# Kernel tuning notes

Hardware: AMD Instinct MI355X
Metric: run time of the kernel (lower is better)

## Reference

```python
import jax, jax.numpy as jnp
import numpy as np
from jax import lax

C = 32          # channel_num
DG = 8          # deformable_groups
K = 9           # 3x3 deformable kernel taps
B, H, W = 4, 192, 192


def conv2d(x, w, b, pad):
    y = lax.conv_general_dilated(x, w, (1, 1), [(pad, pad), (pad, pad)],
                                 dimension_numbers=("NCHW", "OIHW", "NCHW"))
    return y + b[None, :, None, None]


def deform_conv2d(x, offset, mask, w, b):
    """Modulated deformable conv v2, 3x3 kernel, stride 1, pad 1, dilation 1.

    x:      [B, C, H, W]
    offset: [B, 2*DG*K, H, W]  laid out as cat(o1, o2): first DG*K = dy, next = dx
    mask:   [B, DG*K, H, W]    (already sigmoided)
    w:      [Cout, C, 3, 3], b: [Cout]
    """
    Bn, Cn, Hn, Wn = x.shape
    Cg = Cn // DG
    off = offset.reshape(Bn, 2, DG, K, Hn, Wn)
    dy, dx = off[:, 0], off[:, 1]                     # [B, DG, K, H, W]
    m = mask.reshape(Bn, DG, K, Hn, Wn)

    ky = jnp.repeat(jnp.arange(3) - 1, 3).astype(x.dtype)  # [K]
    kx = jnp.tile(jnp.arange(3) - 1, 3).astype(x.dtype)    # [K]
    iy = jnp.arange(Hn, dtype=x.dtype)
    ix = jnp.arange(Wn, dtype=x.dtype)
    py = dy + ky[None, None, :, None, None] + iy[None, None, None, :, None]
    px = dx + kx[None, None, :, None, None] + ix[None, None, None, None, :]

    y0 = jnp.floor(py)
    x0 = jnp.floor(px)
    wy = py - y0    # frac weights
    wx = px - x0

    x_flat = x.reshape(Bn, DG, Cg, Hn * Wn)

    def gather(yc, xc):
        valid = (yc >= 0) & (yc < Hn) & (xc >= 0) & (xc < Wn)
        yi = jnp.clip(yc, 0, Hn - 1).astype(jnp.int32)
        xi = jnp.clip(xc, 0, Wn - 1).astype(jnp.int32)
        idx = (yi * Wn + xi).reshape(Bn, DG, 1, K * Hn * Wn)
        v = jnp.take_along_axis(x_flat, jnp.broadcast_to(idx, (Bn, DG, Cg, K * Hn * Wn)), axis=3)
        v = v.reshape(Bn, DG, Cg, K, Hn, Wn)
        return v * valid[:, :, None].astype(x.dtype)

    v00 = gather(y0, x0)
    v01 = gather(y0, x0 + 1)
    v10 = gather(y0 + 1, x0)
    v11 = gather(y0 + 1, x0 + 1)
    wyb = wy[:, :, None]  # [B, DG, 1, K, H, W]
    wxb = wx[:, :, None]
    sampled = ((1 - wyb) * (1 - wxb) * v00 + (1 - wyb) * wxb * v01
               + wyb * (1 - wxb) * v10 + wyb * wxb * v11)
    sampled = sampled * m[:, :, None]                 # modulate
    sampled = sampled.reshape(Bn, Cn, K, Hn, Wn)      # DG*Cg == C, contiguous
    out = jnp.einsum('oik,bikhw->bohw', w.reshape(w.shape[0], Cn, K), sampled)
    return out + b[None, :, None, None]


def setup_inputs() -> dict:
    key = jax.random.key(0)
    ks = jax.random.split(key, 14)
    f = lambda k, shp, s=1.0: jax.random.normal(k, shp, dtype=jnp.float32) * s
    return {
        "img_ref": f(ks[0], (B, C, H, W)),
        "img": f(ks[1], (B, C, H, W)),
        "conv1_w": f(ks[2], (C, 2 * C, 1, 1), 0.05),
        "conv1_b": f(ks[3], (C,), 0.05),
        "conv2a_w": f(ks[4], (C, C, 3, 3), 0.05),
        "conv2a_b": f(ks[5], (C,), 0.05),
        "conv2b_w": f(ks[6], (C, C, 3, 3), 0.05),
        "conv2b_b": f(ks[7], (C,), 0.05),
        "off_w": f(ks[8], (3 * DG * K, C, 3, 3), 0.01),
        "off_b": f(ks[9], (3 * DG * K,), 0.01),
        "dcn_w": f(ks[10], (C, C, 3, 3), 0.05),
        "dcn_b": f(ks[11], (C,), 0.05),
    }


def reference(img_ref, img, conv1_w, conv1_b, conv2a_w, conv2a_b,
              conv2b_w, conv2b_b, off_w, off_b, dcn_w, dcn_b):
    img_cat = conv2d(jnp.concatenate([img_ref, img], axis=1), conv1_w, conv1_b, 0)
    feat = conv2d(conv2d(img_cat, conv2a_w, conv2a_b, 1), conv2b_w, conv2b_b, 1)
    # DCNv2Pack: offsets/mask from feat, deformable sampling on img
    co = conv2d(feat, off_w, off_b, 1)                # [B, 3*DG*K, H, W]
    o1, o2, mask = jnp.split(co, 3, axis=1)
    offset = jnp.concatenate([o1, o2], axis=1)
    mask = jax.nn.sigmoid(mask)
    return deform_conv2d(img, offset, mask, dcn_w, dcn_b)
```

## Files before the change

### kernel.cpp

```cpp
#include <hip/hip_runtime.h>

#define Hc   192
#define Wc   192
#define HWc  (Hc * Wc)
#define NPIX (4 * HWc)
#define Hp   194
#define Wp   256
#define PLANE (Hp * Wp)

typedef float f32x4 __attribute__((ext_vector_type(4)));
typedef float f32x2 __attribute__((ext_vector_type(2)));
typedef __bf16 bf16x8 __attribute__((ext_vector_type(8)));
typedef unsigned short u16;
typedef unsigned int u32;

#define WF_BO    0
#define WF_B1    224
#define WF_B2A   256
#define WF_B2B   288
#define WF_BD    320
#define FR1_U    0
#define FRA_U    2048
#define FRB_U    11264
#define FRO_U    20480
#define FRD_U    84992
#define FRAG_U_TOT 94208
#define FRAG_BYTE 1408
#define T0_BYTE  (FRAG_BYTE + FRAG_U_TOT * 2)
#define T1_BYTE  (T0_BYTE + NPIX * 32 * 2)
#define IMG_BYTE (T1_BYTE + NPIX * 32 * 2)
#define IMG_SZ   ((size_t)4 * 8 * PLANE * 4 * 2)

__device__ __forceinline__ u16 f2bf(float f) {
    u32 u = __float_as_uint(f);
    u32 r = u + 0x7fffu + ((u >> 16) & 1u);
    return (u16)(r >> 16);
}
__device__ __forceinline__ float bf2f(u16 v) {
    return __uint_as_float(((u32)v) << 16);
}
__device__ __forceinline__ u32 cvtpk(float a, float b) {
    u32 r;
    asm("v_cvt_pk_bf16_f32 %0, %1, %2" : "=v"(r) : "v"(a), "v"(b));
    return r;
}
__device__ __forceinline__ f32x2 unpk(u32 h) {
    return f32x2{__uint_as_float(h << 16), __uint_as_float(h & 0xffff0000u)};
}

__global__ __launch_bounds__(256) void prep_k(
    const float* __restrict__ w1,  const float* __restrict__ b1,
    const float* __restrict__ w2a, const float* __restrict__ b2a,
    const float* __restrict__ w2b, const float* __restrict__ b2b,
    const float* __restrict__ wo,  const float* __restrict__ bo,
    const float* __restrict__ wd,  const float* __restrict__ bd,
    float* __restrict__ wsf, u16* __restrict__ frag)
{
    int i = blockIdx.x * 256 + threadIdx.x;
    if (i < 224)      { wsf[WF_BO + i]  = (i < 216) ? bo[i] : 0.f; return; }
    if (i < 256)      { wsf[WF_B1  + i - 224] = b1[i - 224];  return; }
    if (i < 288)      { wsf[WF_B2A + i - 256] = b2a[i - 256]; return; }
    if (i < 320)      { wsf[WF_B2B + i - 288] = b2b[i - 288]; return; }
    if (i < 352)      { wsf[WF_BD  + i - 320] = bd[i - 320];  return; }
    int fi = i - 352;
    if (fi < 2048) {
        int s = fi >> 10, l = (fi >> 3) & 63, j = fi & 7;
        int nt = (fi >> 9) & 1;
        int o = nt * 16 + (l & 15);
        int ci = s * 32 + ((l >> 4) << 3) + j;
        frag[FR1_U + fi] = f2bf(w1[o * 64 + ci]);
        return;
    }
    fi -= 2048;
    if (fi < 9216) {
        int s = fi / 1024, r = fi - s * 1024;
        int nt = r >> 9, l = (r >> 3) & 63, j = r & 7;
        int o = nt * 16 + (l & 15);
        int ci = ((l >> 4) << 3) + j;
        frag[FRA_U + fi] = f2bf(w2a[(o * 32 + ci) * 9 + s]);
        return;
    }
    fi -= 9216;
    if (fi < 9216) {
        int s = fi / 1024, r = fi - s * 1024;
        int nt = r >> 9, l = (r >> 3) & 63, j = r & 7;
        int o = nt * 16 + (l & 15);
        int ci = ((l >> 4) << 3) + j;
        frag[FRB_U + fi] = f2bf(w2b[(o * 32 + ci) * 9 + s]);
        return;
    }
    fi -= 9216;
    if (fi < 64512) {
        int s = fi / 7168, r = fi - s * 7168;
        int nt = r >> 9, l = (r >> 3) & 63, j = r & 7;
        int o = nt * 16 + (l & 15);
        int ci = ((l >> 4) << 3) + j;
        frag[FRO_U + fi] = f2bf((o < 216) ? wo[(o * 32 + ci) * 9 + s] : 0.f);
        return;
    }
    fi -= 64512;
    if (fi < 9216) {
        int k = fi / 1024, r = fi - k * 1024;
        int nt = r >> 9, l = (r >> 3) & 63, j = r & 7;
        int o = nt * 16 + (l & 15);
        int ci = ((l >> 4) << 3) + j;
        frag[FRD_U + fi] = f2bf(wd[o * 288 + ci * 9 + k]);
        return;
    }
}

__global__ __launch_bounds__(256) void conv1x1_mfma_k(
    const float* __restrict__ f0, const float* __restrict__ f1,
    const u16* __restrict__ wfrag, const float* __restrict__ bias,
    u16* __restrict__ y, u16* __restrict__ dump)
{
    constexpr int M_BLK = 128;
    const int tid = threadIdx.x, lane = tid & 63, wv = tid >> 6;
    const int bid = blockIdx.x;
    const int swz = (bid & 7) * (gridDim.x >> 3) + (bid >> 3);
    const int m0 = swz * M_BLK;
    const int b = m0 / HWc, hwb = m0 - b * HWc;
    const int rm = wv * 32;

    __shared__ uint4 At4[512];

    int pxA[2], hA[2], wA[2], kgA[2];
#pragma unroll
    for (int it = 0; it < 2; ++it) {
        int st = it * 256 + tid;
        int rowl = ((st >> 6) << 4) | (st & 15);
        kgA[it] = (st >> 4) & 3;
        pxA[it] = rowl;
        int hwp = hwb + rowl;
        hA[it] = hwp / Wc;
        wA[it] = hwp - hA[it] * Wc;
    }

    f32x4 acc[2][2];
#pragma unroll
    for (int mf = 0; mf < 2; ++mf)
#pragma unroll
        for (int nf = 0; nf < 2; ++nf)
            acc[mf][nf] = f32x4{0.f, 0.f, 0.f, 0.f};

    for (int s = 0; s < 2; ++s) {
        const float* fs = (s == 0) ? f0 : f1;
#pragma unroll
        for (int it = 0; it < 2; ++it) {
            const float* pl = fs + ((size_t)b * 32 + kgA[it] * 8) * HWc + (hwb + pxA[it]);
            u32 p0, p1, p2, p3;
            {
                u32 a0 = f2bf(pl[0 * HWc]), a1 = f2bf(pl[1 * HWc]);
                u32 a2 = f2bf(pl[2 * HWc]), a3 = f2bf(pl[3 * HWc]);
                u32 a4 = f2bf(pl[4 * HWc]), a5 = f2bf(pl[5 * HWc]);
                u32 a6 = f2bf(pl[6 * HWc]), a7 = f2bf(pl[7 * HWc]);
                p0 = a0 | (a1 << 16); p1 = a2 | (a3 << 16);
                p2 = a4 | (a5 << 16); p3 = a6 | (a7 << 16);
            }
            uint4 v = {p0, p1, p2, p3};
            if (s == 1) {
                size_t base = (((size_t)(b * 8 + kgA[it] * 2)) * PLANE
                               + (size_t)(hA[it] + 1) * Wp + (wA[it] + 2)) * 4;
                *(uint2*)(dump + base) = uint2{p0, p1};
                *(uint2*)(dump + base + (size_t)PLANE * 4) = uint2{p2, p3};
            }
            At4[it * 256 + tid] = v;
        }
        __syncthreads();

        bf16x8 aF[2];
#pragma unroll
        for (int mf = 0; mf < 2; ++mf)
            aF[mf] = __builtin_bit_cast(bf16x8, At4[((rm >> 4) + mf) * 64 + lane]);
#pragma unroll
        for (int nf = 0; nf < 2; ++nf) {
            bf16x8 bF = __builtin_bit_cast(
                bf16x8, *(const uint4*)(wfrag + (((size_t)s * 2 + nf) * 64 + lane) * 8));
#pragma unroll
            for (int mf = 0; mf < 2; ++mf)
                acc[mf][nf] = __builtin_amdgcn_mfma_f32_16x16x32_bf16(aF[mf], bF, acc[mf][nf], 0, 0, 0);
        }
        __syncthreads();
    }

#pragma unroll
    for (int nf = 0; nf < 2; ++nf) {
        int o = nf * 16 + (lane & 15);
        float bs = bias[o];
#pragma unroll
        for (int mf = 0; mf < 2; ++mf) {
#pragma unroll
            for (int r = 0; r < 4; ++r) {
                int m = m0 + rm + mf * 16 + ((lane >> 4) << 2) + r;
                y[(size_t)m * 32 + o] = f2bf(acc[mf][nf][r] + bs);
            }
        }
    }
}

__global__ __launch_bounds__(256, 4) void conv3x3h_k(
    const u16* __restrict__ src,
    const u16* __restrict__ wfrag,
    const float* __restrict__ bias,
    u16* __restrict__ dst)
{
    const int tid = threadIdx.x, lane = tid & 63, wv = tid >> 6;
    const int bid = blockIdx.x;
    const int swz = (bid & 7) * (gridDim.x >> 3) + (bid >> 3);
    const int m0 = swz * 64;
    const int b = m0 / HWc, hwb = m0 - b * HWc;
    const int h0 = hwb / Wc, w0 = hwb - h0 * Wc;

    __shared__ u16 xt[198 * 32];

#pragma unroll
    for (int it = 0; it < 4; ++it) {
        int t = it * 256 + tid;
        if (t < 792) {
            int s = t >> 2, c = t & 3;
            int ry = s / 66, cx = s - ry * 66;
            int row = h0 + ry - 1, col = w0 + cx - 1;
            uint4 v = {0u, 0u, 0u, 0u};
            if (((unsigned)row < (unsigned)Hc) && ((unsigned)col < (unsigned)Wc))
                v = *(const uint4*)(src + ((size_t)(b * HWc + row * Wc + col)) * 32 + c * 8);
            *(uint4*)(xt + (size_t)t * 8) = v;
        }
    }
    __syncthreads();

    f32x4 acc0 = {0.f, 0.f, 0.f, 0.f};
    f32x4 acc1 = {0.f, 0.f, 0.f, 0.f};
    const int r0 = wv * 16 + (lane & 15);
    const int kg8 = (lane >> 4) * 8;
#pragma unroll
    for (int kyi = 0; kyi < 3; ++kyi) {
#pragma unroll
        for (int kxi = 0; kxi < 3; ++kxi) {
            const int s9 = kyi * 3 + kxi;
            bf16x8 aF = __builtin_bit_cast(bf16x8,
                *(const uint4*)(xt + (size_t)(kyi * 66 + r0 + kxi) * 32 + kg8));
            bf16x8 bF0 = __builtin_bit_cast(bf16x8,
                *(const uint4*)(wfrag + (((size_t)s9 * 2 + 0) * 64 + lane) * 8));
            bf16x8 bF1 = __builtin_bit_cast(bf16x8,
                *(const uint4*)(wfrag + (((size_t)s9 * 2 + 1) * 64 + lane) * 8));
            acc0 = __builtin_amdgcn_mfma_f32_16x16x32_bf16(aF, bF0, acc0, 0, 0, 0);
            acc1 = __builtin_amdgcn_mfma_f32_16x16x32_bf16(aF, bF1, acc1, 0, 0, 0);
        }
    }

    const int oL = lane & 15;
    const float bs0 = bias[oL], bs1 = bias[16 + oL];
    u16* dp = dst + (size_t)(m0 + wv * 16 + ((lane >> 4) << 2)) * 32;
#pragma unroll
    for (int r = 0; r < 4; ++r) {
        dp[r * 32 + oL]      = f2bf(acc0[r] + bs0);
        dp[r * 32 + 16 + oL] = f2bf(acc1[r] + bs1);
    }
}

__global__ __launch_bounds__(256, 4) void offdcn_k(
    const u16* __restrict__ t0,
    const u16* __restrict__ imgp,
    const u16* __restrict__ wfragO,
    const u16* __restrict__ wfragD,
    const float* __restrict__ biasO,
    const float* __restrict__ biasD,
    float* __restrict__ out)
{
    const int tid = threadIdx.x, lane = tid & 63, wv = tid >> 6;
    const int bid = blockIdx.x;
    const int swz = (bid & 7) * (gridDim.x >> 3) + (bid >> 3);
    const int m0 = swz * 64;
    const int b = m0 / HWc, hwb = m0 - b * HWc;
    const int h0 = hwb / Wc, w0 = hwb - h0 * Wc;

    __shared__ u16 pool[224 * 66];

    {
        u16* xt = pool;
#pragma unroll
        for (int it = 0; it < 4; ++it) {
            int t = it * 256 + tid;
            if (t < 792) {
                int s = t >> 2, c = t & 3;
                int ry = s / 66, cx = s - ry * 66;
                int row = h0 + ry - 1, col = w0 + cx - 1;
                uint4 v = {0u, 0u, 0u, 0u};
                if (((unsigned)row < (unsigned)Hc) && ((unsigned)col < (unsigned)Wc))
                    v = *(const uint4*)(t0 + ((size_t)(b * HWc + row * Wc + col)) * 32 + c * 8);
                *(uint4*)(xt + (size_t)t * 8) = v;
            }
        }
    }
    __syncthreads();

    const int wm = wv >> 1, wn = wv & 1;
    const int rm = wm * 32, cn = wn * 112;
    f32x4 acc[2][7];
#pragma unroll
    for (int mf = 0; mf < 2; ++mf)
#pragma unroll
        for (int nf = 0; nf < 7; ++nf)
            acc[mf][nf] = f32x4{0.f, 0.f, 0.f, 0.f};
    {
        const u16* xt = pool;
        const int r0 = rm + (lane & 15);
        const int kg8 = (lane >> 4) * 8;
#pragma unroll
        for (int kyi = 0; kyi < 3; ++kyi) {
#pragma unroll
            for (int kxi = 0; kxi < 3; ++kxi) {
                const int s9 = kyi * 3 + kxi;
                bf16x8 aF0 = __builtin_bit_cast(bf16x8,
                    *(const uint4*)(xt + (size_t)(kyi * 66 + r0 + kxi) * 32 + kg8));
                bf16x8 aF1 = __builtin_bit_cast(bf16x8,
                    *(const uint4*)(xt + (size_t)(kyi * 66 + r0 + 16 + kxi) * 32 + kg8));
#pragma unroll
                for (int nf = 0; nf < 7; ++nf) {
                    bf16x8 bF = __builtin_bit_cast(
                        bf16x8,
                        *(const uint4*)(wfragO + (((size_t)s9 * 14 + wn * 7 + nf) * 64 + lane) * 8));
                    acc[0][nf] = __builtin_amdgcn_mfma_f32_16x16x32_bf16(aF0, bF, acc[0][nf], 0, 0, 0);
                    acc[1][nf] = __builtin_amdgcn_mfma_f32_16x16x32_bf16(aF1, bF, acc[1][nf], 0, 0, 0);
                }
            }
        }
    }
    __syncthreads();

    u16* co_s = pool;
#pragma unroll
    for (int nf = 0; nf < 7; ++nf) {
        const int o = cn + nf * 16 + (lane & 15);
        const float bs = biasO[o];
        const bool sig = (o >= 144);
#pragma unroll
        for (int mf = 0; mf < 2; ++mf) {
            const int mb = rm + mf * 16 + ((lane >> 4) << 2);
            float v0 = acc[mf][nf][0] + bs, v1 = acc[mf][nf][1] + bs;
            float v2 = acc[mf][nf][2] + bs, v3 = acc[mf][nf][3] + bs;
            if (sig) {
                v0 = __builtin_amdgcn_rcpf(1.f + __builtin_amdgcn_exp2f(-v0 * 1.44269504f));
                v1 = __builtin_amdgcn_rcpf(1.f + __builtin_amdgcn_exp2f(-v1 * 1.44269504f));
                v2 = __builtin_amdgcn_rcpf(1.f + __builtin_amdgcn_exp2f(-v2 * 1.44269504f));
                v3 = __builtin_amdgcn_rcpf(1.f + __builtin_amdgcn_exp2f(-v3 * 1.44269504f));
            }
            *(u32*)&co_s[o * 66 + mb]     = cvtpk(v0, v1);
            *(u32*)&co_s[o * 66 + mb + 2] = cvtpk(v2, v3);
        }
    }
    __syncthreads();

    {
        const int kg = lane >> 4;
        const int pixb = wv * 16 + (lane & 15);
        const int hw = hwb + pixb;
        const int hh = hw / Wc;
        const int wwp = hw - hh * Wc;
        const float fh = (float)(hh - 1);
        const float fw = (float)(wwp - 1);

        const u16* gb = imgp + (size_t)b * 8 * PLANE * 4;
        const u32 dgp[2] = {(u32)((2 * kg + 0) * (PLANE * 4)),
                            (u32)((2 * kg + 1) * (PLANE * 4))};

        f32x4 acc0 = {0.f, 0.f, 0.f, 0.f};
        f32x4 acc1 = {0.f, 0.f, 0.f, 0.f};

#pragma unroll 1
        for (int kb = 0; kb < 9; kb += 3) {
            float w4[3][2][4];
            uint4 cc[3][2][2];

#pragma unroll
            for (int t = 0; t < 3; ++t) {
                const int k = kb + t;
                const int kyi = k / 3, kxi = k - kyi * 3;
#pragma unroll
                for (int dgi = 0; dgi < 2; ++dgi) {
                    const int offch = (2 * kg + dgi) * 9 + k;
                    float dy = bf2f(co_s[offch * 66 + pixb]);
                    float dx = bf2f(co_s[(72 + offch) * 66 + pixb]);
                    float m  = bf2f(co_s[(144 + offch) * 66 + pixb]);

                    float py = dy + (fh + (float)kyi);
                    float px = dx + (fw + (float)kxi);
                    float y0f = floorf(py), x0f = floorf(px);
                    float wy = py - y0f, wx = px - x0f;
                    int y0 = (int)y0f, x0 = (int)x0f;

                    int yA = min(max(y0 + 1, 0), 193);
                    int yB = min(max(y0 + 2, 0), 193);
                    int xc = min(max(x0 + 2, 0), 254);

                    float wym = wy * m;
                    w4[t][dgi][0] = 1.f - wx;
                    w4[t][dgi][1] = wx;
                    w4[t][dgi][2] = m - wym;
                    w4[t][dgi][3] = wym;

                    u32 rA = dgp[dgi] + ((u32)yA << 10);
                    u32 rB = dgp[dgi] + ((u32)yB << 10);
                    u32 xc4 = (u32)xc << 2;
                    cc[t][dgi][0] = *(const uint4*)(gb + (rA + xc4));
                    cc[t][dgi][1] = *(const uint4*)(gb + (rB + xc4));
                }
            }

#pragma unroll
            for (int t = 0; t < 3; ++t) {
                const int k = kb + t;
                u32 pk[4];
#pragma unroll
                for (int dgi = 0; dgi < 2; ++dgi) {
                    const float w1x = w4[t][dgi][0], wxs = w4[t][dgi][1];
                    const float w1ym = w4[t][dgi][2], wym = w4[t][dgi][3];
                    uint4 tp = cc[t][dgi][0], bt = cc[t][dgi][1];
                    f32x2 t01 = unpk(tp.x) * w1x + unpk(tp.z) * wxs;
                    f32x2 t23 = unpk(tp.y) * w1x + unpk(tp.w) * wxs;
                    f32x2 b01 = unpk(bt.x) * w1x + unpk(bt.z) * wxs;
                    f32x2 b23 = unpk(bt.y) * w1x + unpk(bt.w) * wxs;
                    f32x2 s01 = t01 * w1ym + b01 * wym;
                    f32x2 s23 = t23 * w1ym + b23 * wym;
                    pk[dgi * 2 + 0] = cvtpk(s01.x, s01.y);
                    pk[dgi * 2 + 1] = cvtpk(s23.x, s23.y);
                }

                bf16x8 aF = __builtin_bit_cast(bf16x8, uint4{pk[0], pk[1], pk[2], pk[3]});
                bf16x8 bF0 = __builtin_bit_cast(bf16x8,
                    *(const uint4*)(wfragD + ((size_t)(k * 2 + 0) * 64 + lane) * 8));
                bf16x8 bF1 = __builtin_bit_cast(bf16x8,
                    *(const uint4*)(wfragD + ((size_t)(k * 2 + 1) * 64 + lane) * 8));
                acc0 = __builtin_amdgcn_mfma_f32_16x16x32_bf16(aF, bF0, acc0, 0, 0, 0);
                acc1 = __builtin_amdgcn_mfma_f32_16x16x32_bf16(aF, bF1, acc1, 0, 0, 0);
            }
        }

        const int hw0 = hwb + wv * 16 + ((lane >> 4) << 2);
        float* ob = out + (size_t)b * 32 * HWc;
        const int oL = lane & 15;
        const float bs0 = biasD[oL], bs1 = biasD[16 + oL];
        f32x4 o0 = {acc0[0] + bs0, acc0[1] + bs0, acc0[2] + bs0, acc0[3] + bs0};
        f32x4 o1 = {acc1[0] + bs1, acc1[1] + bs1, acc1[2] + bs1, acc1[3] + bs1};
        *(f32x4*)(ob + (size_t)oL * HWc + hw0) = o0;
        *(f32x4*)(ob + (size_t)(16 + oL) * HWc + hw0) = o1;
    }
}

extern "C" void kernel_launch(void* const* d_in, const int* in_sizes, int n_in,
                              void* d_out, int out_size, void* d_ws, size_t ws_size,
                              hipStream_t stream) {
    const float* img_ref  = (const float*)d_in[0];
    const float* img      = (const float*)d_in[1];
    const float* conv1_w  = (const float*)d_in[2];
    const float* conv1_b  = (const float*)d_in[3];
    const float* conv2a_w = (const float*)d_in[4];
    const float* conv2a_b = (const float*)d_in[5];
    const float* conv2b_w = (const float*)d_in[6];
    const float* conv2b_b = (const float*)d_in[7];
    const float* off_w    = (const float*)d_in[8];
    const float* off_b    = (const float*)d_in[9];
    const float* dcn_w    = (const float*)d_in[10];
    const float* dcn_b    = (const float*)d_in[11];

    float* wsf = (float*)d_ws;
    u16* frag = (u16*)((char*)d_ws + FRAG_BYTE);
    u16* t0   = (u16*)((char*)d_ws + T0_BYTE);
    u16* t1   = (u16*)((char*)d_ws + T1_BYTE);
    u16* imgp = (u16*)((char*)d_ws + IMG_BYTE);
    float* out = (float*)d_out;

    hipMemsetAsync(imgp, 0, IMG_SZ, stream);

    prep_k<<<370, 256, 0, stream>>>(conv1_w, conv1_b, conv2a_w, conv2a_b,
                                    conv2b_w, conv2b_b, off_w, off_b,
                                    dcn_w, dcn_b, wsf, frag);

    conv1x1_mfma_k<<<NPIX / 128, 256, 0, stream>>>(
        img_ref, img, frag + FR1_U, wsf + WF_B1, t0, imgp);

    conv3x3h_k<<<NPIX / 64, 256, 0, stream>>>(t0, frag + FRA_U, wsf + WF_B2A, t1);

    conv3x3h_k<<<NPIX / 64, 256, 0, stream>>>(t1, frag + FRB_U, wsf + WF_B2B, t0);

    offdcn_k<<<NPIX / 64, 256, 0, stream>>>(t0, imgp, frag + FRO_U, frag + FRD_U,
                                            wsf + WF_BO, wsf + WF_BD, out);
}
```

Measured before the change: 97.96 us.

## Software-pipeline deformable gathers, transpose offset tile layout, raise MFMA wave priority

Restructures the deformable sampling loop into a three-stage software pipeline. Gathers for the next tap group are issued before the current group is consumed, with sched barriers keeping that order. The offset/mask tile in shared memory is transposed to a pixel-major layout with stride 216, and the bilinear weights are recomputed in the consume step so fewer registers stay live. s_setprio is raised around the MFMA loops of the conv kernels. The aim is to hide gather latency; the cost is more registers held by two gather buffers, plus scattered 16-bit LDS stores that may cause bank conflicts.

```diff
diff --git a/kernel.cpp b/kernel.cpp
--- a/kernel.cpp
+++ b/kernel.cpp
@@ -232,6 +232,7 @@
     f32x4 acc1 = {0.f, 0.f, 0.f, 0.f};
     const int r0 = wv * 16 + (lane & 15);
     const int kg8 = (lane >> 4) * 8;
+    __builtin_amdgcn_s_setprio(1);
 #pragma unroll
     for (int kyi = 0; kyi < 3; ++kyi) {
 #pragma unroll
@@ -247,6 +248,7 @@
             acc1 = __builtin_amdgcn_mfma_f32_16x16x32_bf16(aF, bF1, acc1, 0, 0, 0);
         }
     }
+    __builtin_amdgcn_s_setprio(0);
 
     const int oL = lane & 15;
     const float bs0 = bias[oL], bs1 = bias[16 + oL];
@@ -274,7 +276,7 @@
     const int b = m0 / HWc, hwb = m0 - b * HWc;
     const int h0 = hwb / Wc, w0 = hwb - h0 * Wc;
 
-    __shared__ u16 pool[224 * 66];
+    __shared__ u16 pool[64 * 216];
 
     {
         u16* xt = pool;
@@ -306,6 +308,7 @@
         const u16* xt = pool;
         const int r0 = rm + (lane & 15);
         const int kg8 = (lane >> 4) * 8;
+        __builtin_amdgcn_s_setprio(1);
 #pragma unroll
         for (int kyi = 0; kyi < 3; ++kyi) {
 #pragma unroll
@@ -325,6 +328,7 @@
                 }
             }
         }
+        __builtin_amdgcn_s_setprio(0);
     }
     __syncthreads();
 
@@ -334,19 +338,24 @@
         const int o = cn + nf * 16 + (lane & 15);
         const float bs = biasO[o];
         const bool sig = (o >= 144);
-#pragma unroll
-        for (int mf = 0; mf < 2; ++mf) {
-            const int mb = rm + mf * 16 + ((lane >> 4) << 2);
-            float v0 = acc[mf][nf][0] + bs, v1 = acc[mf][nf][1] + bs;
-            float v2 = acc[mf][nf][2] + bs, v3 = acc[mf][nf][3] + bs;
-            if (sig) {
-                v0 = __builtin_amdgcn_rcpf(1.f + __builtin_amdgcn_exp2f(-v0 * 1.44269504f));
-                v1 = __builtin_amdgcn_rcpf(1.f + __builtin_amdgcn_exp2f(-v1 * 1.44269504f));
-                v2 = __builtin_amdgcn_rcpf(1.f + __builtin_amdgcn_exp2f(-v2 * 1.44269504f));
-                v3 = __builtin_amdgcn_rcpf(1.f + __builtin_amdgcn_exp2f(-v3 * 1.44269504f));
-            }
-            *(u32*)&co_s[o * 66 + mb]     = cvtpk(v0, v1);
-            *(u32*)&co_s[o * 66 + mb + 2] = cvtpk(v2, v3);
+        if (o < 216) {
+#pragma unroll
+            for (int mf = 0; mf < 2; ++mf) {
+                const int mb = rm + mf * 16 + ((lane >> 4) << 2);
+                float v0 = acc[mf][nf][0] + bs, v1 = acc[mf][nf][1] + bs;
+                float v2 = acc[mf][nf][2] + bs, v3 = acc[mf][nf][3] + bs;
+                if (sig) {
+                    v0 = __builtin_amdgcn_rcpf(1.f + __builtin_amdgcn_exp2f(-v0 * 1.44269504f));
+                    v1 = __builtin_amdgcn_rcpf(1.f + __builtin_amdgcn_exp2f(-v1 * 1.44269504f));
+                    v2 = __builtin_amdgcn_rcpf(1.f + __builtin_amdgcn_exp2f(-v2 * 1.44269504f));
+                    v3 = __builtin_amdgcn_rcpf(1.f + __builtin_amdgcn_exp2f(-v3 * 1.44269504f));
+                }
+                u32 d01 = cvtpk(v0, v1), d23 = cvtpk(v2, v3);
+                co_s[(mb + 0) * 216 + o] = (u16)d01;
+                co_s[(mb + 1) * 216 + o] = (u16)(d01 >> 16);
+                co_s[(mb + 2) * 216 + o] = (u16)d23;
+                co_s[(mb + 3) * 216 + o] = (u16)(d23 >> 16);
+            }
         }
     }
     __syncthreads();
@@ -360,72 +369,65 @@
         const float fh = (float)(hh - 1);
         const float fw = (float)(wwp - 1);
 
+        const u16* cb = co_s + pixb * 216 + kg * 18;
         const u16* gb = imgp + (size_t)b * 8 * PLANE * 4;
-        const u32 dgp[2] = {(u32)((2 * kg + 0) * (PLANE * 4)),
-                            (u32)((2 * kg + 1) * (PLANE * 4))};
+        const u32 dgp0 = (u32)((2 * kg + 0) * (PLANE * 4));
+        const u32 dgp1 = (u32)((2 * kg + 1) * (PLANE * 4));
 
         f32x4 acc0 = {0.f, 0.f, 0.f, 0.f};
         f32x4 acc1 = {0.f, 0.f, 0.f, 0.f};
-
-#pragma unroll 1
-        for (int kb = 0; kb < 9; kb += 3) {
-            float w4[3][2][4];
-            uint4 cc[3][2][2];
-
+        uint4 ccA[3][2][2], ccB[3][2][2];
+
+        auto stage = [&](int kb, uint4 (&cc)[3][2][2]) {
 #pragma unroll
             for (int t = 0; t < 3; ++t) {
                 const int k = kb + t;
                 const int kyi = k / 3, kxi = k - kyi * 3;
 #pragma unroll
                 for (int dgi = 0; dgi < 2; ++dgi) {
-                    const int offch = (2 * kg + dgi) * 9 + k;
-                    float dy = bf2f(co_s[offch * 66 + pixb]);
-                    float dx = bf2f(co_s[(72 + offch) * 66 + pixb]);
-                    float m  = bf2f(co_s[(144 + offch) * 66 + pixb]);
-
+                    float dy = bf2f(cb[dgi * 9 + k]);
+                    float dx = bf2f(cb[72 + dgi * 9 + k]);
                     float py = dy + (fh + (float)kyi);
                     float px = dx + (fw + (float)kxi);
-                    float y0f = floorf(py), x0f = floorf(px);
-                    float wy = py - y0f, wx = px - x0f;
-                    int y0 = (int)y0f, x0 = (int)x0f;
-
+                    int y0 = (int)floorf(py), x0 = (int)floorf(px);
                     int yA = min(max(y0 + 1, 0), 193);
                     int yB = min(max(y0 + 2, 0), 193);
                     int xc = min(max(x0 + 2, 0), 254);
-
-                    float wym = wy * m;
-                    w4[t][dgi][0] = 1.f - wx;
-                    w4[t][dgi][1] = wx;
-                    w4[t][dgi][2] = m - wym;
-                    w4[t][dgi][3] = wym;
-
-                    u32 rA = dgp[dgi] + ((u32)yA << 10);
-                    u32 rB = dgp[dgi] + ((u32)yB << 10);
+                    u32 dgp = dgi ? dgp1 : dgp0;
                     u32 xc4 = (u32)xc << 2;
-                    cc[t][dgi][0] = *(const uint4*)(gb + (rA + xc4));
-                    cc[t][dgi][1] = *(const uint4*)(gb + (rB + xc4));
+                    cc[t][dgi][0] = *(const uint4*)(gb + dgp + ((u32)yA << 10) + xc4);
+                    cc[t][dgi][1] = *(const uint4*)(gb + dgp + ((u32)yB << 10) + xc4);
                 }
             }
-
+        };
+
+        auto consume = [&](int kb, uint4 (&cc)[3][2][2]) {
 #pragma unroll
             for (int t = 0; t < 3; ++t) {
                 const int k = kb + t;
+                const int kyi = k / 3, kxi = k - kyi * 3;
                 u32 pk[4];
 #pragma unroll
                 for (int dgi = 0; dgi < 2; ++dgi) {
-                    const float w1x = w4[t][dgi][0], wxs = w4[t][dgi][1];
-                    const float w1ym = w4[t][dgi][2], wym = w4[t][dgi][3];
+                    float dy = bf2f(cb[dgi * 9 + k]);
+                    float dx = bf2f(cb[72 + dgi * 9 + k]);
+                    float m  = bf2f(cb[144 + dgi * 9 + k]);
+                    float py = dy + (fh + (float)kyi);
+                    float px = dx + (fw + (float)kxi);
+                    float wy = py - floorf(py);
+                    float wx = px - floorf(px);
+                    float wym = wy * m, w1ym = m - wym;
+                    float w1x = 1.f - wx;
                     uint4 tp = cc[t][dgi][0], bt = cc[t][dgi][1];
-                    f32x2 t01 = unpk(tp.x) * w1x + unpk(tp.z) * wxs;
-                    f32x2 t23 = unpk(tp.y) * w1x + unpk(tp.w) * wxs;
-                    f32x2 b01 = unpk(bt.x) * w1x + unpk(bt.z) * wxs;
-                    f32x2 b23 = unpk(bt.y) * w1x + unpk(bt.w) * wxs;
+                    f32x2 t01 = unpk(tp.x) * w1x + unpk(tp.z) * wx;
+                    f32x2 t23 = unpk(tp.y) * w1x + unpk(tp.w) * wx;
+                    f32x2 b01 = unpk(bt.x) * w1x + unpk(bt.z) * wx;
+                    f32x2 b23 = unpk(bt.y) * w1x + unpk(bt.w) * wx;
                     f32x2 s01 = t01 * w1ym + b01 * wym;
                     f32x2 s23 = t23 * w1ym + b23 * wym;
                     pk[dgi * 2 + 0] = cvtpk(s01.x, s01.y);
                     pk[dgi * 2 + 1] = cvtpk(s23.x, s23.y);
                 }
-
                 bf16x8 aF = __builtin_bit_cast(bf16x8, uint4{pk[0], pk[1], pk[2], pk[3]});
                 bf16x8 bF0 = __builtin_bit_cast(bf16x8,
                     *(const uint4*)(wfragD + ((size_t)(k * 2 + 0) * 64 + lane) * 8));
@@ -434,7 +436,16 @@
                 acc0 = __builtin_amdgcn_mfma_f32_16x16x32_bf16(aF, bF0, acc0, 0, 0, 0);
                 acc1 = __builtin_amdgcn_mfma_f32_16x16x32_bf16(aF, bF1, acc1, 0, 0, 0);
             }
-        }
+        };
+
+        stage(0, ccA);
+        stage(3, ccB);
+        __builtin_amdgcn_sched_barrier(0);
+        consume(0, ccA);
+        stage(6, ccA);
+        __builtin_amdgcn_sched_barrier(0);
+        consume(3, ccB);
+        consume(6, ccA);
 
         const int hw0 = hwb + wv * 16 + ((lane >> 4) << 2);
         float* ob = out + (size_t)b * 32 * HWc;
```

New measurement: 106.8 us. 1.09x slower.
